# Optimization experiments

Measured on AMD Instinct MI355X. Metric: run time of the kernel, lower is better.

Reference implementation:

```python
import jax, jax.numpy as jnp
import numpy as np

NUM_EXPERTS = 8
HIDDEN = 2048
INTER = 2048
NUM_TOKENS = 4096
TOP_K = 2


def setup_inputs() -> dict:
    key = jax.random.key(0)
    k1, k2, k3, k4, k5 = jax.random.split(key, 5)
    return {
        "hidden_states": jax.random.normal(k1, (NUM_TOKENS, HIDDEN), jnp.float32),
        "top_k_index": jax.random.randint(k2, (NUM_TOKENS, TOP_K), 0, NUM_EXPERTS),
        "top_k_weights": jax.random.uniform(k3, (NUM_TOKENS, TOP_K), jnp.float32),
        "gate_up_proj": jax.random.normal(k4, (NUM_EXPERTS, 2 * INTER, HIDDEN), jnp.float32),
        "down_proj": jax.random.normal(k5, (NUM_EXPERTS, HIDDEN, INTER), jnp.float32),
    }


def reference(hidden_states, top_k_index, top_k_weights, gate_up_proj, down_proj):
    # hidden_states: [T, H]; top_k_index/weights: [T, K]
    # gate_up_proj: [E, 2I, H]; down_proj: [E, H, I]
    T, H = hidden_states.shape
    K = top_k_index.shape[-1]
    E = gate_up_proj.shape[0]

    # token_idx expansion: [0,0,1,1,...] -> repeat each token K times
    selected = jnp.repeat(hidden_states, K, axis=0)          # [T*K, H]
    expert_ids = top_k_index.reshape(-1)                     # [T*K]
    weights = top_k_weights.reshape(-1)                      # [T*K]

    # Equivalent to sort-by-expert + grouped GEMM + inverse-perm scatter:
    # compute each expert's FFN on all expanded tokens and mask-combine.
    # Same math (order-independent), jit-friendly fixed shapes.
    out = jnp.zeros((T * K, H), dtype=hidden_states.dtype)
    for e in range(E):
        up_gate = selected @ gate_up_proj[e].T               # [T*K, 2I]
        gate, up = jnp.split(up_gate, 2, axis=-1)            # chunk(2, dim=-1)
        act = jax.nn.silu(gate) * up                          # SwiGLU
        down = act @ down_proj[e].T                           # [T*K, H]
        mask = (expert_ids == e).astype(down.dtype)[:, None]
        out = out + mask * down

    out = out * weights[:, None]                              # weighted combine
    return out.reshape(T, K, H).sum(axis=1).astype(hidden_states.dtype)
```

## Files before the change

### kernel.cpp

```cpp
#include <hip/hip_runtime.h>

#define T_TOK 4096
#define HID   2048
#define INTER 2048
#define NEXP  8
#define TK    8192
#define MAXMB 72

typedef __bf16 bf16x8 __attribute__((ext_vector_type(8)));
typedef float  f32x4  __attribute__((ext_vector_type(4)));

__device__ __forceinline__ unsigned short f2bf(float f) {
    unsigned u = __builtin_bit_cast(unsigned, f);
    u += 0x7FFFu + ((u >> 16) & 1u);
    return (unsigned short)(u >> 16);
}

__device__ __forceinline__ void gload_lds16(const unsigned short* g, unsigned short* l) {
    __builtin_amdgcn_global_load_lds(
        (const __attribute__((address_space(1))) unsigned int*)g,
        (__attribute__((address_space(3))) unsigned int*)l,
        16, 0, 0);
}

__global__ void cvt_kernel(const float4* __restrict__ src,
                           ushort4* __restrict__ dst, int n4) {
    int i = blockIdx.x * 256 + threadIdx.x;
    if (i < n4) {
        float4 v = src[i];
        ushort4 o;
        o.x = f2bf(v.x); o.y = f2bf(v.y); o.z = f2bf(v.z); o.w = f2bf(v.w);
        dst[i] = o;
    }
}

__global__ void route_kernel(const int* __restrict__ topk,
                             int* __restrict__ offsets,
                             int* __restrict__ sorted,
                             int* __restrict__ btab,
                             int* __restrict__ nbt) {
    __shared__ int cnt[NEXP];
    __shared__ int pos[NEXP];
    int tid = threadIdx.x;
    if (tid < NEXP) cnt[tid] = 0;
    __syncthreads();
    for (int i = tid; i < TK; i += 256) atomicAdd(&cnt[topk[i]], 1);
    __syncthreads();
    if (tid == 0) {
        int s = 0;
        for (int e = 0; e < NEXP; e++) { offsets[e] = s; pos[e] = s; s += cnt[e]; }
        offsets[NEXP] = s;
        int nb = 0;
        for (int e = 0; e < NEXP; e++) {
            int nmb = (cnt[e] + 127) >> 7;
            for (int m = 0; m < nmb; m++) btab[nb++] = (e << 16) | m;
        }
        nbt[0] = nb;
    }
    __syncthreads();
    for (int i = tid; i < TK; i += 256) {
        int e = topk[i];
        int p = atomicAdd(&pos[e], 1);
        sorted[p] = i;
    }
}

template <int MODE>
__global__ __launch_bounds__(256, 3)
void moe_gemm(const unsigned short* __restrict__ A_src,
              const unsigned short* __restrict__ W,
              const int* __restrict__ offsets,
              const int* __restrict__ sorted,
              const float* __restrict__ wts,
              const int* __restrict__ btab,
              const int* __restrict__ nbt,
              unsigned short* __restrict__ act,
              float* __restrict__ out) {
    constexpr int KD = 2048;
    constexpr int NW = (MODE == 0) ? 4096 : 2048;

    const int bx = blockIdx.x;
    if (bx >= nbt[0]) return;
    const int ent = btab[bx];
    const int e   = ent >> 16;
    const int off = offsets[e];
    const int cnt = offsets[e + 1] - off;
    const int m0  = (ent & 0xffff) * 128;
    const int n0  = blockIdx.y * ((MODE == 0) ? 64 : 128);
    const unsigned short* Wb = W + (size_t)e * NW * KD;

    __shared__ unsigned short Asm[128 * 64];
    __shared__ unsigned short Bsm[128 * 64];
    __shared__ int rowid[128];

    const int tid = threadIdx.x;
    if (tid < 128) {
        int gm = m0 + tid;
        if (MODE == 0) rowid[tid] = (gm < cnt) ? (sorted[off + gm] >> 1) : 0;
        else           rowid[tid] = off + ((gm < cnt) ? gm : (cnt - 1));
    }
    __syncthreads();

    const int wave = tid >> 6, lane = tid & 63;
    const int quad = lane >> 4, lrow = lane & 15;
    const int wm = wave >> 1, wn = wave & 1;
    const int wv1 = wave & 1, wv2 = wave >> 1;

    const int srow = wv1 * 64 + lane;
    const int arid = rowid[srow];
    int wr;
    if (MODE == 0) wr = n0 + wv1 * 32 + (lane & 31) + (lane >> 5) * 2048;
    else           wr = n0 + srow;

    const unsigned short* aptr[4];
    const unsigned short* bptr[4];
    unsigned short* adst[4];
    unsigned short* bdst[4];
#pragma unroll
    for (int c = 0; c < 4; c++) {
        int k8 = 2 * c + wv2;
        aptr[c] = A_src + (size_t)arid * 2048 + k8 * 8;
        bptr[c] = Wb + (size_t)wr * 2048 + k8 * 8;
        adst[c] = &Asm[(k8 * 128 + wv1 * 64) * 8];
        bdst[c] = &Bsm[(k8 * 128 + wv1 * 64) * 8];
    }

    const unsigned short* a_rd = &Asm[(quad * 128 + wm * 64 + lrow) * 8];
    const unsigned short* b_rd = &Bsm[(quad * 128 + wn * 64 + lrow) * 8];

    f32x4 acc[4][4];
#pragma unroll
    for (int i = 0; i < 4; i++)
#pragma unroll
        for (int j = 0; j < 4; j++) acc[i][j] = (f32x4){0.f, 0.f, 0.f, 0.f};

    for (int k0 = 0; k0 < KD; k0 += 64) {
#pragma unroll
        for (int c = 0; c < 4; c++) {
            gload_lds16(aptr[c] + k0, adst[c]);
            gload_lds16(bptr[c] + k0, bdst[c]);
        }
        __syncthreads();

#pragma unroll
        for (int ks = 0; ks < 2; ks++) {
            bf16x8 af[4], bfr[4];
#pragma unroll
            for (int mt = 0; mt < 4; mt++)
                af[mt] = *(const bf16x8*)(a_rd + ks * 4096 + mt * 128);
#pragma unroll
            for (int nt = 0; nt < 4; nt++)
                bfr[nt] = *(const bf16x8*)(b_rd + ks * 4096 + nt * 128);
#pragma unroll
            for (int mt = 0; mt < 4; mt++)
#pragma unroll
                for (int nt = 0; nt < 4; nt++)
                    acc[mt][nt] = __builtin_amdgcn_mfma_f32_16x16x32_bf16(
                        af[mt], bfr[nt], acc[mt][nt], 0, 0, 0);
        }
        __syncthreads();
    }

    if (MODE == 0) {
#pragma unroll
        for (int mt = 0; mt < 4; mt++) {
#pragma unroll
            for (int r = 0; r < 4; r++) {
                int gm = m0 + wm * 64 + mt * 16 + quad * 4 + r;
                if (gm < cnt) {
                    unsigned short* arow = act + (size_t)(off + gm) * 2048;
#pragma unroll
                    for (int nt = 0; nt < 2; nt++) {
                        int col = n0 + wn * 32 + nt * 16 + lrow;
                        float g = acc[mt][nt][r];
                        float u = acc[mt][nt + 2][r];
                        float s = g / (1.f + __expf(-g));
                        arow[col] = f2bf(s * u);
                    }
                }
            }
        }
    } else {
#pragma unroll
        for (int mt = 0; mt < 4; mt++) {
#pragma unroll
            for (int r = 0; r < 4; r++) {
                int gm = m0 + wm * 64 + mt * 16 + quad * 4 + r;
                if (gm < cnt) {
                    int idx = sorted[off + gm];
                    float w = wts[idx];
                    float* orow = out + (size_t)(idx >> 1) * HID;
#pragma unroll
                    for (int nt = 0; nt < 4; nt++) {
                        int n = n0 + wn * 64 + nt * 16 + lrow;
                        atomicAdd(orow + n, w * acc[mt][nt][r]);
                    }
                }
            }
        }
    }
}

extern "C" void kernel_launch(void* const* d_in, const int* in_sizes, int n_in,
                              void* d_out, int out_size, void* d_ws, size_t ws_size,
                              hipStream_t stream) {
    const float* x    = (const float*)d_in[0];
    const int*   topk = (const int*)d_in[1];
    const float* wts  = (const float*)d_in[2];
    const float* Wgu  = (const float*)d_in[3];
    const float* Wd   = (const float*)d_in[4];
    float* out = (float*)d_out;

    char* ws = (char*)d_ws;
    int* offsets = (int*)ws;
    int* sorted  = offsets + 16;
    int* btab    = offsets + 8208;
    int* nbt     = offsets + 8336;
    unsigned short* Wgu_bf = (unsigned short*)(ws + 65536);
    unsigned short* Wd_bf  = Wgu_bf;
    unsigned short* x_bf   = (unsigned short*)(ws + 65536 + (size_t)NEXP * 2 * INTER * HID * 2);
    unsigned short* act    = x_bf + (size_t)T_TOK * HID;

    hipMemsetAsync(d_out, 0, (size_t)out_size * sizeof(float), stream);

    cvt_kernel<<<(T_TOK * HID / 4) / 256, 256, 0, stream>>>(
        (const float4*)x, (ushort4*)x_bf, T_TOK * HID / 4);
    cvt_kernel<<<(NEXP * 2 * INTER * HID / 4) / 256, 256, 0, stream>>>(
        (const float4*)Wgu, (ushort4*)Wgu_bf, NEXP * 2 * INTER * HID / 4);

    route_kernel<<<1, 256, 0, stream>>>(topk, offsets, sorted, btab, nbt);

    moe_gemm<0><<<dim3(MAXMB, 32), 256, 0, stream>>>(
        x_bf, Wgu_bf, offsets, sorted, wts, btab, nbt, act, nullptr);

    cvt_kernel<<<(NEXP * HID * INTER / 4) / 256, 256, 0, stream>>>(
        (const float4*)Wd, (ushort4*)Wd_bf, NEXP * HID * INTER / 4);

    moe_gemm<1><<<dim3(MAXMB, 16), 256, 0, stream>>>(
        act, Wd_bf, offsets, sorted, wts, btab, nbt, nullptr, out);
}
```

Before: 1.103 ms.

## Enlarge MoE GEMM tiles to 256 rows with 512 threads and double-buffered LDS

The grouped GEMM tile grows from 128x128 to 256x256 (gate/up) or 256x256 (down) with 8 waves per block. Global-to-LDS loads are double-buffered so the next K-slice is fetched while MFMAs run on the current one. The routing table now uses 256-row blocks, and the grid is remapped so neighbouring blocks spread across experts. This targets more operand reuse per loaded byte and hides load latency, at the cost of 128KB of LDS per block, fewer blocks in flight, and more padded rows for partially filled expert tiles.

```diff
diff --git a/kernel.cpp b/kernel.cpp
--- a/kernel.cpp
+++ b/kernel.cpp
@@ -5,7 +5,8 @@
 #define INTER 2048
 #define NEXP  8
 #define TK    8192
-#define MAXMB 72
+#define MAXMB 40
+#define NT    32
 
 typedef __bf16 bf16x8 __attribute__((ext_vector_type(8)));
 typedef float  f32x4  __attribute__((ext_vector_type(4)));
@@ -52,7 +53,7 @@
         offsets[NEXP] = s;
         int nb = 0;
         for (int e = 0; e < NEXP; e++) {
-            int nmb = (cnt[e] + 127) >> 7;
+            int nmb = (cnt[e] + 255) >> 8;
             for (int m = 0; m < nmb; m++) btab[nb++] = (e << 16) | m;
         }
         nbt[0] = nb;
@@ -66,7 +67,7 @@
 }
 
 template <int MODE>
-__global__ __launch_bounds__(256, 3)
+__global__ __launch_bounds__(512, 2)
 void moe_gemm(const unsigned short* __restrict__ A_src,
               const unsigned short* __restrict__ W,
               const int* __restrict__ offsets,
@@ -76,25 +77,25 @@
               const int* __restrict__ nbt,
               unsigned short* __restrict__ act,
               float* __restrict__ out) {
-    constexpr int KD = 2048;
-    constexpr int NW = (MODE == 0) ? 4096 : 2048;
-
-    const int bx = blockIdx.x;
+    constexpr int KD    = 2048;
+    constexpr int NWROW = (MODE == 0) ? 4096 : 2048;
+
+    const int bx = (blockIdx.x & 7) * (MAXMB / 8) + (blockIdx.x >> 3);
     if (bx >= nbt[0]) return;
     const int ent = btab[bx];
     const int e   = ent >> 16;
     const int off = offsets[e];
     const int cnt = offsets[e + 1] - off;
-    const int m0  = (ent & 0xffff) * 128;
-    const int n0  = blockIdx.y * ((MODE == 0) ? 64 : 128);
-    const unsigned short* Wb = W + (size_t)e * NW * KD;
-
-    __shared__ unsigned short Asm[128 * 64];
-    __shared__ unsigned short Bsm[128 * 64];
-    __shared__ int rowid[128];
+    const int m0  = (ent & 0xffff) * 256;
+    const int n0  = blockIdx.y * ((MODE == 0) ? 128 : 256);
+    const unsigned short* Wb = W + (size_t)e * NWROW * KD;
+
+    __shared__ unsigned short Asm[2][16384];
+    __shared__ unsigned short Bsm[2][16384];
+    __shared__ int rowid[256];
 
     const int tid = threadIdx.x;
-    if (tid < 128) {
+    if (tid < 256) {
         int gm = m0 + tid;
         if (MODE == 0) rowid[tid] = (gm < cnt) ? (sorted[off + gm] >> 1) : 0;
         else           rowid[tid] = off + ((gm < cnt) ? gm : (cnt - 1));
@@ -103,77 +104,81 @@
 
     const int wave = tid >> 6, lane = tid & 63;
     const int quad = lane >> 4, lrow = lane & 15;
-    const int wm = wave >> 1, wn = wave & 1;
-    const int wv1 = wave & 1, wv2 = wave >> 1;
-
-    const int srow = wv1 * 64 + lane;
-    const int arid = rowid[srow];
-    int wr;
-    if (MODE == 0) wr = n0 + wv1 * 32 + (lane & 31) + (lane >> 5) * 2048;
-    else           wr = n0 + srow;
-
-    const unsigned short* aptr[4];
-    const unsigned short* bptr[4];
-    unsigned short* adst[4];
-    unsigned short* bdst[4];
+    const int wm = wave >> 2, wn = wave & 3;
+
+    const unsigned short* asrc[4];
+    const unsigned short* bsrc[4];
+    int dstoff[4];
 #pragma unroll
     for (int c = 0; c < 4; c++) {
-        int k8 = 2 * c + wv2;
-        aptr[c] = A_src + (size_t)arid * 2048 + k8 * 8;
-        bptr[c] = Wb + (size_t)wr * 2048 + k8 * 8;
-        adst[c] = &Asm[(k8 * 128 + wv1 * 64) * 8];
-        bdst[c] = &Bsm[(k8 * 128 + wv1 * 64) * 8];
-    }
-
-    const unsigned short* a_rd = &Asm[(quad * 128 + wm * 64 + lrow) * 8];
-    const unsigned short* b_rd = &Bsm[(quad * 128 + wn * 64 + lrow) * 8];
-
-    f32x4 acc[4][4];
-#pragma unroll
-    for (int i = 0; i < 4; i++)
+        int r = c * 64 + lane;
+        asrc[c] = A_src + (size_t)rowid[r] * KD + wave * 8;
+        int wr;
+        if (MODE == 0) wr = n0 + (r >> 5) * 16 + (r & 15) + ((r >> 4) & 1) * 2048;
+        else           wr = n0 + r;
+        bsrc[c] = Wb + (size_t)wr * KD + wave * 8;
+        dstoff[c] = (wave * 256 + c * 64) * 8;
+    }
+
+    const int ardoff = (quad * 256 + wm * 128 + lrow) * 8;
+    const int brdoff = (quad * 256 + wn * 64 + lrow) * 8;
+
+    f32x4 acc[8][4];
+#pragma unroll
+    for (int i = 0; i < 8; i++)
 #pragma unroll
         for (int j = 0; j < 4; j++) acc[i][j] = (f32x4){0.f, 0.f, 0.f, 0.f};
 
-    for (int k0 = 0; k0 < KD; k0 += 64) {
+    auto STAGE = [&](int buf, int k0) {
 #pragma unroll
         for (int c = 0; c < 4; c++) {
-            gload_lds16(aptr[c] + k0, adst[c]);
-            gload_lds16(bptr[c] + k0, bdst[c]);
-        }
-        __syncthreads();
-
-#pragma unroll
-        for (int ks = 0; ks < 2; ks++) {
-            bf16x8 af[4], bfr[4];
-#pragma unroll
-            for (int mt = 0; mt < 4; mt++)
-                af[mt] = *(const bf16x8*)(a_rd + ks * 4096 + mt * 128);
+            gload_lds16(asrc[c] + k0, &Asm[buf][dstoff[c]]);
+            gload_lds16(bsrc[c] + k0, &Bsm[buf][dstoff[c]]);
+        }
+    };
+
+    STAGE(0, 0);
+    __syncthreads();
+
+    int cur = 0;
+    for (int t = 0; t < NT; ++t) {
+        if (t + 1 < NT) STAGE(cur ^ 1, (t + 1) * 64);
+
+        const unsigned short* a0 = &Asm[cur][ardoff];
+        const unsigned short* b0 = &Bsm[cur][brdoff];
+#pragma unroll
+        for (int ks = 0; ks < 2; ++ks) {
+            bf16x8 af[8], bfr[4];
+#pragma unroll
+            for (int mt = 0; mt < 8; mt++)
+                af[mt] = *(const bf16x8*)(a0 + ks * 8192 + mt * 128);
 #pragma unroll
             for (int nt = 0; nt < 4; nt++)
-                bfr[nt] = *(const bf16x8*)(b_rd + ks * 4096 + nt * 128);
-#pragma unroll
-            for (int mt = 0; mt < 4; mt++)
+                bfr[nt] = *(const bf16x8*)(b0 + ks * 8192 + nt * 128);
+#pragma unroll
+            for (int mt = 0; mt < 8; mt++)
 #pragma unroll
                 for (int nt = 0; nt < 4; nt++)
                     acc[mt][nt] = __builtin_amdgcn_mfma_f32_16x16x32_bf16(
                         af[mt], bfr[nt], acc[mt][nt], 0, 0, 0);
         }
         __syncthreads();
+        cur ^= 1;
     }
 
     if (MODE == 0) {
 #pragma unroll
-        for (int mt = 0; mt < 4; mt++) {
+        for (int mt = 0; mt < 8; mt++) {
 #pragma unroll
             for (int r = 0; r < 4; r++) {
-                int gm = m0 + wm * 64 + mt * 16 + quad * 4 + r;
+                int gm = m0 + wm * 128 + mt * 16 + quad * 4 + r;
                 if (gm < cnt) {
                     unsigned short* arow = act + (size_t)(off + gm) * 2048;
 #pragma unroll
-                    for (int nt = 0; nt < 2; nt++) {
-                        int col = n0 + wn * 32 + nt * 16 + lrow;
-                        float g = acc[mt][nt][r];
-                        float u = acc[mt][nt + 2][r];
+                    for (int p = 0; p < 2; p++) {
+                        int col = n0 + wn * 32 + p * 16 + lrow;
+                        float g = acc[mt][2 * p][r];
+                        float u = acc[mt][2 * p + 1][r];
                         float s = g / (1.f + __expf(-g));
                         arow[col] = f2bf(s * u);
                     }
@@ -182,10 +187,10 @@
         }
     } else {
 #pragma unroll
-        for (int mt = 0; mt < 4; mt++) {
+        for (int mt = 0; mt < 8; mt++) {
 #pragma unroll
             for (int r = 0; r < 4; r++) {
-                int gm = m0 + wm * 64 + mt * 16 + quad * 4 + r;
+                int gm = m0 + wm * 128 + mt * 16 + quad * 4 + r;
                 if (gm < cnt) {
                     int idx = sorted[off + gm];
                     float w = wts[idx];
@@ -230,12 +235,12 @@
 
     route_kernel<<<1, 256, 0, stream>>>(topk, offsets, sorted, btab, nbt);
 
-    moe_gemm<0><<<dim3(MAXMB, 32), 256, 0, stream>>>(
+    moe_gemm<0><<<dim3(MAXMB, 16), 512, 0, stream>>>(
         x_bf, Wgu_bf, offsets, sorted, wts, btab, nbt, act, nullptr);
 
     cvt_kernel<<<(NEXP * HID * INTER / 4) / 256, 256, 0, stream>>>(
         (const float4*)Wd, (ushort4*)Wd_bf, NEXP * HID * INTER / 4);
 
-    moe_gemm<1><<<dim3(MAXMB, 16), 256, 0, stream>>>(
+    moe_gemm<1><<<dim3(MAXMB, 8), 512, 0, stream>>>(
         act, Wd_bf, offsets, sorted, wts, btab, nbt, nullptr, out);
 }
```

Result: slower. 1.167 ms (+5.8%).
